# Optimization experiments

Hardware: AMD Instinct MI355X
Metric: run time of the kernel (lower is better)

Reference implementation:

```python
import jax, jax.numpy as jnp
import numpy as np
from jax import lax

K = 3          # kernel (patch size)
D = 64         # MPO bond dimension
F = K * K      # feature dim per patch (k^2 * C, C=1)
S = F          # output-index spacing inside each SMPO
OUT = 10       # final output dimension
B = 128        # batch size
H = 81         # image height = width
SIGMA = 1e-3   # 'random_eye' noise scale


def patch_embed(x, k=K):
    """squeeze_image + trigonometric embedding.
    x: (B, h, w) -> unit vectors (B, N, 2) with N=(h/k)*(w/k).
    Each k*k patch row is embedded as the L2-normalized mean of
    [cos(pi/2 x), sin(pi/2 x)] over its k^2 features."""
    b, h, w = x.shape
    p = x.reshape(b, h // k, k, w // k, k).transpose(0, 1, 3, 2, 4)
    p = p.reshape(b, (h // k) * (w // k), k * k)
    ang = 0.5 * jnp.pi * p
    v = jnp.stack([jnp.cos(ang).mean(-1), jnp.sin(ang).mean(-1)], axis=-1)
    return v / jnp.linalg.norm(v, axis=-1, keepdims=True)


def smpo_layer(v, W_out, W_mid):
    """Spaced MPO applied to a product-state MPS, read out per output site.
    v:      (B, n, 2)  input site vectors (n = J*S sites, output at every S-th)
    W_out:  (J, D, D, 2, F)  output-site tensors (identity baseline baked in)
    W_mid:  (J, S-1, D, D, 2) non-output site tensors; effective matrix is
            M = I + einsum('bp,dep->bde', v, W) ('random_eye' init).
    Output row j = L_j . A_j(v) . R_j where L/R are left/right chain
    environments with the other output indices closed with ones.
    Returns (B, J, F)."""
    b, n, _ = v.shape
    J = W_out.shape[0]
    s = n // J
    eye = jnp.eye(D, dtype=v.dtype)
    vg = v.reshape(b, J, s, 2)
    v_out = vg[:, :, 0, :].transpose(1, 0, 2)        # (J, B, 2)
    v_mid = vg[:, :, 1:, :].transpose(1, 2, 0, 3)    # (J, S-1, B, 2)

    def left_step(l, xs):
        A, vo, Wm, vm = xs
        Lj = l                                       # env left of output site j
        l = jnp.einsum('bd,bp,depf->be', l, vo, A)   # Abar (f summed = ones closure)
        for t in range(s - 1):
            M = eye + jnp.einsum('bp,dep->bde', vm[t], Wm[t])
            l = jnp.einsum('bd,bde->be', l, M)
        return l, Lj

    def right_step(r, xs):
        A, vo, Wm, vm = xs
        for t in reversed(range(s - 1)):
            M = eye + jnp.einsum('bp,dep->bde', vm[t], Wm[t])
            r = jnp.einsum('bde,be->bd', M, r)
        Rj = r                                       # env right of output site j
        r = jnp.einsum('bp,depf,be->bd', vo, A, r)
        return r, Rj

    bnd = jnp.zeros((b, D), v.dtype).at[:, 0].set(1.0)  # bond-1 boundary
    xs = (W_out, v_out, W_mid, v_mid)
    _, L = lax.scan(jax.checkpoint(left_step), bnd, xs)
    _, R = lax.scan(jax.checkpoint(right_step), bnd, xs, reverse=True)
    return jnp.einsum('jbd,jdepf,jbp,jbe->bjf', L, W_out, v_out, R)


def final_layer(x, A0, W_mid):
    """Final SMPO (spacing = n, single output index at site 0), fully
    contracted left-to-right. x: (B, n) -> (B, OUT)."""
    ang = 0.5 * jnp.pi * x
    v = jnp.stack([jnp.cos(ang), jnp.sin(ang)], axis=-1)   # (B, n, 2)
    eye = jnp.eye(D, dtype=x.dtype)
    u = jnp.einsum('bp,epo->beo', v[:, 0], A0[0])          # left boundary e0

    def step(u, xs):
        Wm, vm = xs
        M = eye + jnp.einsum('bp,dep->bde', vm, Wm)
        return jnp.einsum('bdo,bde->beo', u, M), None

    u, _ = lax.scan(jax.checkpoint(step), u, (W_mid, v[:, 1:].transpose(1, 0, 2)))
    return u[:, 0, :]                                      # right boundary e0


def setup_inputs() -> dict:
    key = jax.random.key(0)
    ks = jax.random.split(key, 7)
    eyeD = np.eye(D, dtype=np.float32)

    def wout(k, J):  # identity baseline + noise ('random_eye')
        base = jnp.asarray((0.8 / F) * eyeD[:, :, None, None])
        return base + SIGMA * jax.random.normal(k, (J, D, D, 2, F), jnp.float32)

    def wmid(k, J):
        return SIGMA * jax.random.normal(k, (J, S - 1, D, D, 2), jnp.float32)

    x = jax.random.uniform(ks[0], (B, H, H, 1), jnp.float32)
    Wout0 = wout(ks[1], 81)
    Wmid0 = wmid(ks[2], 81)
    Wout1 = wout(ks[3], 9)
    Wmid1 = wmid(ks[4], 9)
    A0f = jnp.asarray(0.1 * eyeD[:, :, None, None]) + SIGMA * jax.random.normal(
        ks[5], (D, D, 2, OUT), jnp.float32)
    WmidF = SIGMA * jax.random.normal(ks[6], (80, D, D, 2), jnp.float32)
    return {"x": x, "Wout0": Wout0, "Wmid0": Wmid0, "Wout1": Wout1,
            "Wmid1": Wmid1, "A0f": A0f, "WmidF": WmidF}


def reference(x, Wout0, Wmid0, Wout1, Wmid1, A0f, WmidF):
    v0 = patch_embed(x[..., 0])                    # (B, 729, 2)
    h1 = smpo_layer(v0, Wout0, Wmid0)              # (B, 81, 9)
    v1 = patch_embed(h1.reshape(-1, 27, 27))       # (B, 81, 2)
    h2 = smpo_layer(v1, Wout1, Wmid1)              # (B, 9, 9)
    return final_layer(h2.reshape(-1, 81), A0f, WmidF)  # (B, 10)
```

## Files before the change

### kernel.cpp

```cpp
#include <hip/hip_runtime.h>
#include <cstdint>
#include <cstddef>


typedef float    f32x16 __attribute__((ext_vector_type(16)));
typedef _Float16 f16x8  __attribute__((ext_vector_type(8)));
typedef __fp16   fp16x2 __attribute__((ext_vector_type(2)));
typedef _Float16 h2_t   __attribute__((ext_vector_type(2)));
typedef unsigned int uint32x2_t __attribute__((ext_vector_type(2)));
typedef const void __attribute__((address_space(1))) gas_t;
typedef void       __attribute__((address_space(3))) las_t;

union U16  { uint4 u; f16x8 h; };
union B16u { uint32_t u[4]; f16x8 h; };
union H2U  { fp16x2 h; uint32_t u; };

__device__ __forceinline__ uint32_t pkf16(float a, float b){
  H2U z; z.h = __builtin_amdgcn_cvt_pkrtz(a, b); return z.u;
}
__device__ __forceinline__ uint32_t pkmul(uint32_t a, uint32_t b){
  H2U x, y, r; x.u = a; y.u = b;
  r.h = x.h * y.h; return r.u;
}
__device__ __forceinline__ uint32_t packh2(float a, float b){
  union { _Float16 h[2]; uint32_t u; } z;
  z.h[0] = (_Float16)a; z.h[1] = (_Float16)b; return z.u;
}
__device__ __forceinline__ float fdot2f(uint32_t wa, uint32_t wb, float acc){
  union U { uint32_t u; h2_t h; };
  U a, b; a.u = wa; b.u = wb;
  return __builtin_amdgcn_fdot2(a.h, b.h, acc, false);
}

#define REC 17408

__global__ void k_build(const float* __restrict__ Wmid, const float* __restrict__ Wout,
                        char* __restrict__ S, int J, int n, int dirR){
  int tid = blockIdx.x*256 + threadIdx.x;
  if (tid >= n*4096) return;
  int gt = tid >> 12, r = tid & 4095;
  int f = r >> 8, ln = (r >> 2) & 63, dw = r & 3;
  int s = f >> 1, m = f & 1;
  int row = m*32 + (ln & 31);
  int kb = s*16 + (ln >> 5)*8 + dw*2;
  int p = kb >> 6, q = kb & 63;
  int jj = gt/9, pos = gt - jj*9;
  int j = dirR ? (J-1-jj) : jj;
  int outs = dirR ? 8 : 0;
  float w[2];
  #pragma unroll
  for (int k2 = 0; k2 < 2; ++k2){
    int qq = q + k2;
    int d = dirR ? row : qq;
    int e = dirR ? qq : row;
    float val;
    if (pos == outs){
      const float* src = Wout + ((((size_t)j*64 + d)*64 + e)*2 + p)*9;
      val = 0.f;
      #pragma unroll
      for (int ff = 0; ff < 9; ++ff) val += src[ff];
      if (d == e) val -= 0.8f;
    } else {
      int mi = dirR ? (7 - pos) : (pos - 1);
      val = Wmid[((((size_t)j*8 + mi)*64 + d)*64 + e)*2 + p];
    }
    w[k2] = val;
  }
  uint32_t* S32 = (uint32_t*)(S + (size_t)gt*REC);
  S32[f*256 + ln*4 + dw] = packh2(w[0]*256.f, w[1]*256.f);
}

__global__ void k_buildF(const float* __restrict__ Wm, char* __restrict__ S){
  int tid = blockIdx.x*256 + threadIdx.x;
  if (tid >= 80*4096) return;
  int gt = tid >> 12, r = tid & 4095;
  int f = r >> 8, ln = (r >> 2) & 63, dw = r & 3;
  int s = f >> 1, m = f & 1;
  int row = m*32 + (ln & 31);
  int kb = s*16 + (ln >> 5)*8 + dw*2;
  int p = kb >> 6, q = kb & 63;
  float w[2];
  #pragma unroll
  for (int k2 = 0; k2 < 2; ++k2){
    int d = q + k2, e = row;
    w[k2] = Wm[(((size_t)gt*64 + d)*64 + e)*2 + p];
  }
  uint32_t* S32 = (uint32_t*)(S + (size_t)gt*REC);
  S32[f*256 + ln*4 + dw] = packh2(w[0]*256.f, w[1]*256.f);
}

__global__ void k_vrec(const float2* __restrict__ v, char* __restrict__ S,
                       int n, int nv, int mode){
  int tid = blockIdx.x*256 + threadIdx.x;
  if (tid >= n*128) return;
  int gt = tid >> 7, b = tid & 127;
  int site = (mode == 0) ? gt : (mode == 1) ? (n-1-gt) : (gt+1);
  *(float2*)(S + (size_t)gt*REC + 16384 + b*8) = v[(size_t)b*nv + site];
}

__global__ void k_embed(const float* __restrict__ img, int Wd, int PG,
                        float2* __restrict__ outv){
  int tid = blockIdx.x*256 + threadIdx.x;
  int NP = PG*PG;
  if (tid >= 128*NP) return;
  int b = tid / NP, s = tid - b*NP;
  int pi = s / PG, pj = s - pi*PG;
  const float* base = img + (size_t)b*Wd*Wd + (size_t)(3*pi)*Wd + 3*pj;
  float cs = 0.f, sn = 0.f;
  #pragma unroll
  for (int r = 0; r < 3; ++r){
    #pragma unroll
    for (int c = 0; c < 3; ++c){
      float x = base[r*Wd + c];
      float s_, c_; sincosf(1.5707963267948966f*x, &s_, &c_);
      cs += c_; sn += s_;
    }
  }
  cs *= (1.f/9.f); sn *= (1.f/9.f);
  float rn = rsqrtf(cs*cs + sn*sn);
  float2 v; v.x = cs*rn; v.y = sn*rn;
  outv[tid] = v;
}

__device__ __forceinline__ void stage17(const char* g, char* l){
  #pragma unroll
  for (int i = 0; i < 17; ++i)
    __builtin_amdgcn_global_load_lds((gas_t*)(const void*)(g + i*1024),
                                     (las_t*)(void*)(l + i*1024), 16, 0, 0);
}

#define MKBASE(acc, bd) do { \
  uint32_t P0 = pkf16(acc[0],acc[1]),  P1 = pkf16(acc[2],acc[3]); \
  uint32_t P2 = pkf16(acc[4],acc[5]),  P3 = pkf16(acc[6],acc[7]); \
  { uint32x2_t r_ = __builtin_amdgcn_permlane32_swap(P0, P2, false, false); \
    bd[0] = r_[0]; bd[2] = r_[1]; } \
  { uint32x2_t r_ = __builtin_amdgcn_permlane32_swap(P1, P3, false, false); \
    bd[1] = r_[0]; bd[3] = r_[1]; } \
  uint32_t R0 = pkf16(acc[8],acc[9]),   R1 = pkf16(acc[10],acc[11]); \
  uint32_t R2 = pkf16(acc[12],acc[13]), R3 = pkf16(acc[14],acc[15]); \
  { uint32x2_t r_ = __builtin_amdgcn_permlane32_swap(R0, R2, false, false); \
    bd[4] = r_[0]; bd[6] = r_[1]; } \
  { uint32x2_t r_ = __builtin_amdgcn_permlane32_swap(R1, R3, false, false); \
    bd[5] = r_[0]; bd[7] = r_[1]; } \
} while(0)

#define MFMA8(slotp) do { \
  const uint4* fr_ = (const uint4*)(slotp); \
  _Pragma("unroll") \
  for (int s_ = 0; s_ < 8; ++s_){ \
    const int sl_ = s_ & 3; \
    const uint32_t* bb_ = (sl_ < 2) ? bd0 : bd1; \
    const int off_ = (sl_ & 1)*4; \
    const uint32_t scl_ = (s_ < 4) ? px : py; \
    B16u bs_; \
    _Pragma("unroll") \
    for (int dw_ = 0; dw_ < 4; ++dw_) bs_.u[dw_] = pkmul(bb_[off_+dw_], scl_); \
    U16 fa0_, fa1_; \
    fa0_.u = fr_[(2*s_)*64 + ln]; \
    fa1_.u = fr_[(2*s_+1)*64 + ln]; \
    acc0 = __builtin_amdgcn_mfma_f32_32x32x16_f16(fa0_.h, bs_.h, acc0, 0, 0, 0); \
    acc1 = __builtin_amdgcn_mfma_f32_32x32x16_f16(fa1_.h, bs_.h, acc1, 0, 0, 0); \
  } \
} while(0)

#define PROD_SLOOP(buf) do { \
  const uint4* fr = (const uint4*)(buf); \
  _Pragma("unroll") \
  for (int s = 0; s < 8; ++s){ \
    const int sl = s & 3; \
    const uint32_t scl = (s < 4) ? px : py; \
    const int off = (sl & 1)*4; \
    U16 f0, f1; \
    f0.u = fr[(2*s)*64 + ln]; \
    f1.u = fr[(2*s+1)*64 + ln]; \
    { \
      const uint32_t* bb = (sl < 2) ? bl0 : bh0; \
      B16u bs; \
      _Pragma("unroll") \
      for (int dw = 0; dw < 4; ++dw) bs.u[dw] = pkmul(bb[off+dw], scl); \
      a00 = __builtin_amdgcn_mfma_f32_32x32x16_f16(f0.h, bs.h, a00, 0, 0, 0); \
      a10 = __builtin_amdgcn_mfma_f32_32x32x16_f16(f1.h, bs.h, a10, 0, 0, 0); \
    } \
    { \
      const uint32_t* bb = (sl < 2) ? bl1 : bh1; \
      B16u bs; \
      _Pragma("unroll") \
      for (int dw = 0; dw < 4; ++dw) bs.u[dw] = pkmul(bb[off+dw], scl); \
      a01 = __builtin_amdgcn_mfma_f32_32x32x16_f16(f0.h, bs.h, a01, 0, 0, 0); \
      a11 = __builtin_amdgcn_mfma_f32_32x32x16_f16(f1.h, bs.h, a11, 0, 0, 0); \
    } \
  } \
} while(0)

#define PROD_INIT_I() do { \
  _Pragma("unroll") \
  for (int i = 0; i < 16; ++i){ a00[i]=0.f; a01[i]=0.f; a10[i]=0.f; a11[i]=0.f; } \
  if (((i32 >> 2) & 1) == h){ \
    int rr0 = (i32 & 3) | ((i32 >> 3) << 2); \
    _Pragma("unroll") \
    for (int rr = 0; rr < 16; ++rr) \
      if (rr == rr0){ a00[rr] = 1.f; a11[rr] = 1.f; } \
  } \
} while(0)

#define PROD_WRITEOUT(ob, diagc) do { \
  _Pragma("unroll") \
  for (int x = 0; x < 2; ++x){ \
    _Pragma("unroll") \
    for (int y = 0; y < 2; ++y){ \
      const f32x16& A = (x==0) ? (y==0 ? a00 : a01) : (y==0 ? a10 : a11); \
      int C = y*32 + i32; \
      _Pragma("unroll") \
      for (int r = 0; r < 16; ++r){ \
        int R = x*32 + (r & 3) + 8*(r >> 2) + 4*h; \
        float val = (A[r] - ((R == C) ? (diagc) : 0.f))*256.f; \
        float oth = __shfl_xor(val, 1); \
        if (!(ln & 1)){ \
          uint32_t dwv = packh2(val, oth); \
          *(uint32_t*)((ob) + R*128 + ((C*2) ^ ((R & 7) << 4))) = dwv; \
        } \
      } \
    } \
  } \
} while(0)

#define PROD_STEP(t, doalpha) do { \
  uint32_t px = pkf16(vv[t].x*INV, vv[t].x*INV); \
  uint32_t py = pkf16(vv[t].y*INV, vv[t].y*INV); \
  uint32_t bl0[8], bh0[8], bl1[8], bh1[8]; \
  MKBASE(a00, bl0); MKBASE(a10, bh0); \
  MKBASE(a01, bl1); MKBASE(a11, bh1); \
  if (doalpha){ \
    _Pragma("unroll") \
    for (int i = 0; i < 16; ++i){ \
      a00[i] *= alphaC; a01[i] *= alphaC; a10[i] *= alphaC; a11[i] *= alphaC; \
    } \
  } \
  PROD_SLOOP(lds + (size_t)(t)*16384); \
} while(0)

__global__ __launch_bounds__(512, 1) void k_prod(
    const char* __restrict__ sL, const char* __restrict__ sR,
    const float2* __restrict__ v, char* __restrict__ Tn, char* __restrict__ Wn,
    int J){
  __shared__ __align__(16) char lds[9*16384];
  const int ln = threadIdx.x & 63, w = threadIdx.x >> 6;
  const int wid = (blockIdx.x & 7)*(J*4) + (blockIdx.x >> 3);
  const int bg = wid & 15;
  const int pair = wid >> 4;
  const int dir = pair & 1, j = pair >> 1;
  const int b = bg*8 + w;
  const int h = ln >> 5, i32 = ln & 31;
  const float INV = 1.f/256.f;
  const char* stream = dir ? sR : sL;
  const int n = J*9;

  float2 vv[9];
  {
    const float2* vbase = v + (size_t)b*n + j*9;
    #pragma unroll
    for (int t = 0; t < 9; ++t) vv[t] = vbase[dir ? (9 - t) : t];
  }
  const float alphaC = (dir && j == J-1) ? 1.0f : 0.8f*(vv[0].x + vv[0].y);
  if (dir && j == J-1){ vv[0].x = 0.f; vv[0].y = 0.f; }

  auto gtf = [&](int t) -> int {
    int g = dir ? ((J-2-j)*9 + 8 + t) : (j*9 + t);
    return g < 0 ? 0 : g;
  };
  auto stage = [&](int t){
    const char* g0 = stream + (size_t)gtf(t)*REC + (size_t)(2*w)*1024 + (size_t)ln*16;
    char* l0 = lds + (size_t)t*16384;
    __builtin_amdgcn_global_load_lds((gas_t*)(const void*)g0,
                                     (las_t*)(void*)(l0 + 2*w*1024), 16, 0, 0);
    __builtin_amdgcn_global_load_lds((gas_t*)(const void*)(g0 + 1024),
                                     (las_t*)(void*)(l0 + (2*w+1)*1024), 16, 0, 0);
  };

  f32x16 a00, a01, a10, a11;
  PROD_INIT_I();

  stage(0); stage(1); stage(2);
  asm volatile("s_waitcnt vmcnt(0)" ::: "memory");
  __builtin_amdgcn_s_barrier();
  #pragma unroll
  for (int t = 3; t < 9; ++t) stage(t);

  PROD_STEP(0, true);
  PROD_STEP(1, false);
  PROD_STEP(2, false);
  asm volatile("s_waitcnt vmcnt(0)" ::: "memory");
  __builtin_amdgcn_s_barrier();
  #pragma unroll
  for (int t = 3; t < 9; ++t) PROD_STEP(t, false);

  char* ob = (dir ? Wn : Tn) + ((size_t)b*J + j)*8192;
  PROD_WRITEOUT(ob, alphaC);
}

__global__ __launch_bounds__(512, 1) void k_prodF(
    const char* __restrict__ sF, const float2* __restrict__ vF,
    char* __restrict__ GF){
  __shared__ __align__(16) char lds[8*16384];
  const int ln = threadIdx.x & 63, w = threadIdx.x >> 6;
  const int wid = (blockIdx.x & 7)*20 + (blockIdx.x >> 3);
  const int bg = wid & 15, g = wid >> 4;
  const int b = bg*8 + w;
  const int h = ln >> 5, i32 = ln & 31;
  const float INV = 1.f/256.f;
  const float alphaC = 1.0f;

  float2 vv[8];
  {
    const float2* vbase = vF + (size_t)b*81 + g*8 + 1;
    #pragma unroll
    for (int t = 0; t < 8; ++t) vv[t] = vbase[t];
  }
  auto stage = [&](int t){
    const char* g0 = sF + (size_t)(g*8 + t)*REC + (size_t)(2*w)*1024 + (size_t)ln*16;
    char* l0 = lds + (size_t)t*16384;
    __builtin_amdgcn_global_load_lds((gas_t*)(const void*)g0,
                                     (las_t*)(void*)(l0 + 2*w*1024), 16, 0, 0);
    __builtin_amdgcn_global_load_lds((gas_t*)(const void*)(g0 + 1024),
                                     (las_t*)(void*)(l0 + (2*w+1)*1024), 16, 0, 0);
  };

  f32x16 a00, a01, a10, a11;
  PROD_INIT_I();

  stage(0); stage(1); stage(2);
  asm volatile("s_waitcnt vmcnt(0)" ::: "memory");
  __builtin_amdgcn_s_barrier();
  #pragma unroll
  for (int t = 3; t < 8; ++t) stage(t);

  PROD_STEP(0, false);
  PROD_STEP(1, false);
  PROD_STEP(2, false);
  asm volatile("s_waitcnt vmcnt(0)" ::: "memory");
  __builtin_amdgcn_s_barrier();
  #pragma unroll
  for (int t = 3; t < 8; ++t) PROD_STEP(t, false);

  char* ob = GF + ((size_t)b*10 + g)*8192;
  PROD_WRITEOUT(ob, 1.0f);
}

__global__ __launch_bounds__(64, 1) void k_gscan(
    const char* __restrict__ Tn, const char* __restrict__ Wn,
    const float2* __restrict__ v,
    float* __restrict__ Lout, float* __restrict__ Rout, int J){
  __shared__ __align__(16) char slot[4][8192];
  __shared__ __align__(16) float2 vvs[81];
  __shared__ __align__(16) uint32_t pk32[32];
  const int ln = threadIdx.x;
  const int dir = blockIdx.x >> 7;
  const int b = blockIdx.x & 127;
  const float INV = 1.f/256.f;
  const char* P = (dir ? Wn : Tn) + (size_t)b*J*8192;

  for (int g = ln; g < J; g += 64) vvs[g] = v[(size_t)b*(J*9) + (size_t)g*9];

  auto JD = [&](int g){ return dir ? (J-1-g) : g; };
  auto stage8 = [&](int jx, int sl){
    const char* g0 = P + (size_t)jx*8192 + (size_t)ln*16;
    #pragma unroll
    for (int i = 0; i < 8; ++i)
      __builtin_amdgcn_global_load_lds((gas_t*)(const void*)(g0 + i*1024),
                                       (las_t*)(void*)(slot[sl] + i*1024), 16, 0, 0);
  };

  stage8(JD(0), 0);
  stage8(JD(1 < J-1 ? 1 : J-1), 1);
  stage8(JD(2 < J-1 ? 2 : J-1), 2);

  float st = (ln == 0) ? 1.f : 0.f;
  const uint32_t swz = (uint32_t)(ln & 7) << 4;

  #pragma unroll 1
  for (int g = 0; g < J; ++g){
    const int j = JD(g);
    asm volatile("s_waitcnt vmcnt(16)" ::: "memory");
    if (!dir) Lout[((size_t)j*128 + b)*64 + ln] = st;
    {
      int gn = (g+3 > J-1) ? (J-1) : (g+3);
      stage8(JD(gn), (g+3) & 3);
    }

    float c;
    if (dir) c = (j < J-1) ? 0.8f*(vvs[j+1].x + vvs[j+1].y) : 1.0f;
    else     c = 0.8f*(vvs[j].x + vvs[j].y);

    {
      float o = __shfl_xor(st, 1);
      pk32[ln>>1] = (ln & 1) ? packh2(o, st) : packh2(st, o);
    }
    const char* sp = slot[g & 3] + (size_t)ln*128;
    const uint4* lp = (const uint4*)pk32;
    float acc = 0.f;
    #pragma unroll
    for (int m = 0; m < 8; ++m){
      uint4 q = lp[m];
      uint4 ww = *(const uint4*)(sp + ((m*16) ^ swz));
      acc = fdot2f(ww.x, q.x, acc); acc = fdot2f(ww.y, q.y, acc);
      acc = fdot2f(ww.z, q.z, acc); acc = fdot2f(ww.w, q.w, acc);
    }
    st = c*st + acc*INV;
    if (dir) Rout[((size_t)j*128 + b)*64 + ln] = st;
  }
}

__global__ __launch_bounds__(64, 1) void k_fscan(
    const char* __restrict__ GF, const float* __restrict__ A0f,
    const float2* __restrict__ vF, float* __restrict__ outp){
  __shared__ __align__(16) char slot[4][8192];
  __shared__ __align__(16) uint32_t pk[10][32];
  const int ln = threadIdx.x;
  const int b = blockIdx.x;
  const float INV = 1.f/256.f;
  const char* P = GF + (size_t)b*10*8192;

  float2 v0 = vF[(size_t)b*81];
  float u[10];
  #pragma unroll
  for (int o = 0; o < 10; ++o)
    u[o] = v0.x*A0f[(ln*2+0)*10 + o] + v0.y*A0f[(ln*2+1)*10 + o];

  auto stage8 = [&](int g, int sl){
    const char* g0 = P + (size_t)g*8192 + (size_t)ln*16;
    #pragma unroll
    for (int i = 0; i < 8; ++i)
      __builtin_amdgcn_global_load_lds((gas_t*)(const void*)(g0 + i*1024),
                                       (las_t*)(void*)(slot[sl] + i*1024), 16, 0, 0);
  };

  stage8(0, 0);
  stage8(1, 1);
  stage8(2, 2);
  const uint32_t swz = (uint32_t)(ln & 7) << 4;

  #pragma unroll 1
  for (int g = 0; g < 10; ++g){
    asm volatile("s_waitcnt vmcnt(16)" ::: "memory");
    {
      int gn = (g+3 > 9) ? 9 : (g+3);
      stage8(gn, (g+3) & 3);
    }
    #pragma unroll
    for (int o = 0; o < 10; ++o){
      float ot = __shfl_xor(u[o], 1);
      pk[o][ln>>1] = (ln & 1) ? packh2(ot, u[o]) : packh2(u[o], ot);
    }
    const char* sp = slot[g & 3] + (size_t)ln*128;
    uint4 wr[8];
    #pragma unroll
    for (int m = 0; m < 8; ++m) wr[m] = *(const uint4*)(sp + ((m*16) ^ swz));
    #pragma unroll
    for (int o = 0; o < 10; ++o){
      const uint4* lp = (const uint4*)pk[o];
      float acc = 0.f;
      #pragma unroll
      for (int m = 0; m < 8; ++m){
        uint4 q = lp[m];
        acc = fdot2f(wr[m].x, q.x, acc); acc = fdot2f(wr[m].y, q.y, acc);
        acc = fdot2f(wr[m].z, q.z, acc); acc = fdot2f(wr[m].w, q.w, acc);
      }
      u[o] += acc*INV;
    }
  }
  if (ln == 0){
    #pragma unroll
    for (int o = 0; o < 10; ++o) outp[(size_t)b*10 + o] = u[o];
  }
}

__global__ __launch_bounds__(64, 1) void k_scan_m(
    const char* __restrict__ sL, const char* __restrict__ sR,
    float* __restrict__ Lout, float* __restrict__ Rout, int J, int n){
  __shared__ __align__(16) char lds[4*REC];
  const int ln = threadIdx.x;
  const int wg = blockIdx.x;
  const int dir = wg >> 2;
  const int colbase = (wg & 3)*32;
  const char* stream = dir ? sR : sL;
  float* Sout = dir ? Rout : Lout;
  const int outs = dir ? 8 : 0;
  const int b = colbase + (ln & 31);
  const int h4 = (ln >> 5)*4;
  const float INV = 1.f/256.f;

  f32x16 acc0, acc1;
  #pragma unroll
  for (int i = 0; i < 16; ++i){ acc0[i] = 0.f; acc1[i] = 0.f; }
  if (ln < 32) acc0[0] = 1.f;

  const char* gsrc = stream + (size_t)ln*16;
  stage17(gsrc,           lds);
  stage17(gsrc + REC,     lds + REC);
  stage17(gsrc + 2*REC,   lds + 2*REC);

  int pos = 0, jj = 0;
  for (int t = 0; t < n; ++t){
    asm volatile("s_waitcnt vmcnt(34)" ::: "memory");
    const char* slot = lds + (size_t)(t & 3)*REC;
    float2 vv = *(const float2*)(slot + 16384 + b*8);
    int tn = t + 3; if (tn > n-1) tn = n-1;
    stage17(gsrc + (size_t)tn*REC, lds + (size_t)(tn & 3)*REC);

    uint32_t px = pkf16(vv.x*INV, vv.x*INV);
    uint32_t py = pkf16(vv.y*INV, vv.y*INV);
    uint32_t bd0[8], bd1[8];
    MKBASE(acc0, bd0);
    MKBASE(acc1, bd1);

    if (pos == outs){
      int jdx = dir ? (J-1-jj) : jj;
      float* dst = Sout + ((size_t)jdx*128 + b)*64;
      #pragma unroll
      for (int q = 0; q < 4; ++q){
        float4 f0; f0.x = acc0[4*q]; f0.y = acc0[4*q+1]; f0.z = acc0[4*q+2]; f0.w = acc0[4*q+3];
        *(float4*)(dst + 8*q + h4) = f0;
        float4 f1; f1.x = acc1[4*q]; f1.y = acc1[4*q+1]; f1.z = acc1[4*q+2]; f1.w = acc1[4*q+3];
        *(float4*)(dst + 32 + 8*q + h4) = f1;
      }
      float alpha = 0.8f*(vv.x + vv.y);
      #pragma unroll
      for (int i = 0; i < 16; ++i){ acc0[i] *= alpha; acc1[i] *= alpha; }
    }

    MFMA8(slot);

    ++pos; if (pos == 9){ pos = 0; ++jj; }
  }
}

__global__ __launch_bounds__(64, 1) void k_final_m(
    const char* __restrict__ sF, const float* __restrict__ A0f,
    const float2* __restrict__ vF, float* __restrict__ outp){
  __shared__ __align__(16) char lds[4*REC];
  const int ln = threadIdx.x;
  const int wg = blockIdx.x;
  const int o = wg >> 2;
  const int b = (wg & 3)*32 + (ln & 31);
  const int h4 = (ln >> 5)*4;
  const float INV = 1.f/256.f;

  float2 v0 = vF[(size_t)b*81];
  f32x16 acc0, acc1;
  #pragma unroll
  for (int rg = 0; rg < 16; ++rg){
    int row0 = (rg & 3) + 8*(rg >> 2) + h4;
    acc0[rg] = v0.x*A0f[(row0*2+0)*10 + o] + v0.y*A0f[(row0*2+1)*10 + o];
    int row1 = row0 + 32;
    acc1[rg] = v0.x*A0f[(row1*2+0)*10 + o] + v0.y*A0f[(row1*2+1)*10 + o];
  }
  asm volatile("s_waitcnt vmcnt(0)" ::: "memory");

  const char* gsrc = sF + (size_t)ln*16;
  stage17(gsrc,         lds);
  stage17(gsrc + REC,   lds + REC);
  stage17(gsrc + 2*REC, lds + 2*REC);

  const int n = 80;
  for (int t = 0; t < n; ++t){
    asm volatile("s_waitcnt vmcnt(34)" ::: "memory");
    const char* slot = lds + (size_t)(t & 3)*REC;
    float2 vv = *(const float2*)(slot + 16384 + b*8);
    int tn = t + 3; if (tn > n-1) tn = n-1;
    stage17(gsrc + (size_t)tn*REC, lds + (size_t)(tn & 3)*REC);

    uint32_t px = pkf16(vv.x*INV, vv.x*INV);
    uint32_t py = pkf16(vv.y*INV, vv.y*INV);
    uint32_t bd0[8], bd1[8];
    MKBASE(acc0, bd0);
    MKBASE(acc1, bd1);
    MFMA8(slot);
  }
  if (ln < 32) outp[(size_t)b*10 + o] = acc0[0];
}

template<bool EMB>
__global__ __launch_bounds__(256) void k_out(
    const float* __restrict__ Wout, const float* __restrict__ Lbuf,
    const float* __restrict__ Rbuf, const float2* __restrict__ v, int n,
    float* __restrict__ hout, float2* __restrict__ vF){
  __shared__ float tile[8][64][20];
  __shared__ float Lsh[32][65];
  const int j = blockIdx.x, bh = blockIdx.y;
  const int q = threadIdx.x >> 5, bl = threadIdx.x & 31;
  const int b = bh*32 + bl;
  for (int idx = threadIdx.x; idx < 32*64; idx += 256){
    int r = idx >> 6, d = idx & 63;
    Lsh[r][d] = Lbuf[((size_t)j*128 + bh*32 + r)*64 + d];
  }
  float Rr[8];
  {
    const float4* Rp = (const float4*)(Rbuf + ((size_t)j*128 + b)*64 + q*8);
    ((float4*)Rr)[0] = Rp[0];
    ((float4*)Rr)[1] = Rp[1];
  }
  float acc[18];
  #pragma unroll
  for (int k = 0; k < 18; ++k) acc[k] = 0.f;
  __syncthreads();
  for (int c = 0; c < 8; ++c){
    #pragma unroll
    for (int k = 0; k < 2; ++k){
      int pi = threadIdx.x*2 + k;
      int d8 = pi >> 6, e = pi & 63;
      const float* src = Wout + ((size_t)(j*64 + c*8 + d8)*64 + e)*18;
      float* dst = &tile[d8][e][0];
      #pragma unroll
      for (int mm = 0; mm < 18; ++mm) dst[mm] = src[mm];
    }
    __syncthreads();
    #pragma unroll 1
    for (int d8 = 0; d8 < 8; ++d8){
      float lw = Lsh[bl][c*8 + d8];
      #pragma unroll
      for (int i = 0; i < 8; ++i){
        int e = q*8 + i;
        float wbe = lw * Rr[i];
        const float* tp = &tile[d8][e][0];
        float4 t0 = *(const float4*)(tp);
        float4 t1 = *(const float4*)(tp+4);
        float4 t2 = *(const float4*)(tp+8);
        float4 t3 = *(const float4*)(tp+12);
        float2 t4 = *(const float2*)(tp+16);
        acc[0]  += wbe*t0.x; acc[1]  += wbe*t0.y; acc[2]  += wbe*t0.z; acc[3]  += wbe*t0.w;
        acc[4]  += wbe*t1.x; acc[5]  += wbe*t1.y; acc[6]  += wbe*t1.z; acc[7]  += wbe*t1.w;
        acc[8]  += wbe*t2.x; acc[9]  += wbe*t2.y; acc[10] += wbe*t2.z; acc[11] += wbe*t2.w;
        acc[12] += wbe*t3.x; acc[13] += wbe*t3.y; acc[14] += wbe*t3.z; acc[15] += wbe*t3.w;
        acc[16] += wbe*t4.x; acc[17] += wbe*t4.y;
      }
    }
    __syncthreads();
  }
  float* red = &tile[0][0][0];
  #pragma unroll
  for (int k = 0; k < 18; ++k) red[((size_t)q*32 + bl)*20 + k] = acc[k];
  __syncthreads();
  if (q == 0){
    float s[18];
    #pragma unroll
    for (int k = 0; k < 18; ++k){
      float t = 0.f;
      #pragma unroll
      for (int g = 0; g < 8; ++g) t += red[((size_t)g*32 + bl)*20 + k];
      s[k] = t;
    }
    float2 vo = v[(size_t)b*n + j*9];
    #pragma unroll
    for (int f = 0; f < 9; ++f){
      float val = vo.x*s[f] + vo.y*s[9+f];
      if (EMB){
        float s_, c_; sincosf(1.5707963267948966f*val, &s_, &c_);
        float2 e2; e2.x = c_; e2.y = s_;
        vF[(size_t)b*81 + j*9 + f] = e2;
      } else {
        hout[(size_t)b*729 + j*9 + f] = val;
      }
    }
  }
}

extern "C" void kernel_launch(void* const* d_in, const int* in_sizes, int n_in,
                              void* d_out, int out_size, void* d_ws, size_t ws_size,
                              hipStream_t stream){
  const float* x     = (const float*)d_in[0];
  const float* Wout0 = (const float*)d_in[1];
  const float* Wmid0 = (const float*)d_in[2];
  const float* Wout1 = (const float*)d_in[3];
  const float* Wmid1 = (const float*)d_in[4];
  const float* A0f   = (const float*)d_in[5];
  const float* WmidF = (const float*)d_in[6];
  float* outp = (float*)d_out;

  char* ws = (char*)d_ws;
  size_t off = 0;
  auto alloc = [&](size_t bytes) -> char* {
    char* p = ws + off;
    off = (off + bytes + 255) & ~(size_t)255;
    return p;
  };
  char* S0L = alloc((size_t)729*REC);
  char* S0R = alloc((size_t)729*REC);
  char* S1L = alloc((size_t)81*REC);
  char* S1R = alloc((size_t)81*REC);
  char* SF  = alloc((size_t)80*REC);
  float2* v0 = (float2*)alloc((size_t)128*729*8);
  float2* v1 = (float2*)alloc((size_t)128*81*8);
  float2* vF = (float2*)alloc((size_t)128*81*8);
  float* L0 = (float*)alloc((size_t)81*128*64*4);
  float* R0 = (float*)alloc((size_t)81*128*64*4);
  float* L1 = (float*)alloc((size_t)9*128*64*4);
  float* R1 = (float*)alloc((size_t)9*128*64*4);
  float* h1 = (float*)alloc((size_t)128*729*4);
  char* Tn1 = alloc((size_t)128*81*8192);
  char* Wn1 = alloc((size_t)128*81*8192);
  size_t need_r7 = off;
  char* Tn2 = alloc((size_t)128*9*8192);
  char* Wn2 = alloc((size_t)128*9*8192);
  char* GF  = alloc((size_t)128*10*8192);
  size_t need_full = off;
  bool full = (ws_size >= need_full);
  bool grp1 = (ws_size >= need_r7);
  (void)in_sizes; (void)n_in; (void)out_size;

  k_build <<<1296,  256, 0, stream>>>(Wmid1, Wout1, S1L, 9, 81, 0);
  k_build <<<1296,  256, 0, stream>>>(Wmid1, Wout1, S1R, 9, 81, 1);
  k_buildF<<<1280,  256, 0, stream>>>(WmidF, SF);
  k_build<<<11664, 256, 0, stream>>>(Wmid0, Wout0, S0L, 81, 729, 0);
  k_build<<<11664, 256, 0, stream>>>(Wmid0, Wout0, S0R, 81, 729, 1);

  k_embed<<<365, 256, 0, stream>>>(x, 81, 27, v0);
  if (grp1){
    k_prod <<<2592, 512, 0, stream>>>(S0L, S0R, v0, Tn1, Wn1, 81);
    k_gscan<<<256, 64, 0, stream>>>(Tn1, Wn1, v0, L0, R0, 81);
  } else {
    k_vrec <<<365, 256, 0, stream>>>(v0, S0L, 729, 729, 0);
    k_vrec <<<365, 256, 0, stream>>>(v0, S0R, 729, 729, 1);
    k_scan_m<<<8, 64, 0, stream>>>(S0L, S0R, L0, R0, 81, 729);
  }
  k_out<false><<<dim3(81,4), 256, 0, stream>>>(Wout0, L0, R0, v0, 729, h1, (float2*)nullptr);

  k_embed<<<41, 256, 0, stream>>>(h1, 27, 9, v1);
  if (full){
    k_prod <<<288, 512, 0, stream>>>(S1L, S1R, v1, Tn2, Wn2, 9);
    k_gscan<<<256, 64, 0, stream>>>(Tn2, Wn2, v1, L1, R1, 9);
  } else {
    k_vrec <<<41, 256, 0, stream>>>(v1, S1L, 81, 81, 0);
    k_vrec <<<41, 256, 0, stream>>>(v1, S1R, 81, 81, 1);
    k_scan_m<<<8, 64, 0, stream>>>(S1L, S1R, L1, R1, 9, 81);
  }
  k_out<true><<<dim3(9,4), 256, 0, stream>>>(Wout1, L1, R1, v1, 81, (float*)nullptr, vF);

  if (full){
    k_prodF<<<160, 512, 0, stream>>>(SF, vF, GF);
    k_fscan<<<128, 64, 0, stream>>>(GF, A0f, vF, outp);
  } else {
    k_vrec <<<40, 256, 0, stream>>>(vF, SF, 80, 81, 2);
    k_final_m<<<40, 64, 0, stream>>>(SF, A0f, vF, outp);
  }
}
```

Measured before the change: 502.6 us.

## Replace full-LDS staging with a 3-slot ring buffer in product kernels

The product kernels now stage weight tiles through a 3-slot LDS ring with prefetch distance 2 and a per-step waitcnt and barrier. Before, they staged all 8 or 9 tiles into LDS in two bulk phases. This cuts LDS use per block from 144KB to 48KB and overlaps each load with compute more evenly. In exchange it adds a barrier every step and issues redundant loads of the last tile at the tail. Launch bounds still force one block per SM, so the lower LDS use does not raise occupancy.

```diff
diff --git a/kernel.cpp b/kernel.cpp
--- a/kernel.cpp
+++ b/kernel.cpp
@@ -224,7 +224,7 @@
   } \
 } while(0)
 
-#define PROD_STEP(t, doalpha) do { \
+#define PROD_STEP(t, doalpha, bufp) do { \
   uint32_t px = pkf16(vv[t].x*INV, vv[t].x*INV); \
   uint32_t py = pkf16(vv[t].y*INV, vv[t].y*INV); \
   uint32_t bl0[8], bh0[8], bl1[8], bh1[8]; \
@@ -236,14 +236,14 @@
       a00[i] *= alphaC; a01[i] *= alphaC; a10[i] *= alphaC; a11[i] *= alphaC; \
     } \
   } \
-  PROD_SLOOP(lds + (size_t)(t)*16384); \
+  PROD_SLOOP(bufp); \
 } while(0)
 
 __global__ __launch_bounds__(512, 1) void k_prod(
     const char* __restrict__ sL, const char* __restrict__ sR,
     const float2* __restrict__ v, char* __restrict__ Tn, char* __restrict__ Wn,
     int J){
-  __shared__ __align__(16) char lds[9*16384];
+  __shared__ __align__(16) char lds[3][16384];
   const int ln = threadIdx.x & 63, w = threadIdx.x >> 6;
   const int wid = (blockIdx.x & 7)*(J*4) + (blockIdx.x >> 3);
   const int bg = wid & 15;
@@ -268,31 +268,30 @@
     int g = dir ? ((J-2-j)*9 + 8 + t) : (j*9 + t);
     return g < 0 ? 0 : g;
   };
-  auto stage = [&](int t){
+  auto stage = [&](int t, int sl){
     const char* g0 = stream + (size_t)gtf(t)*REC + (size_t)(2*w)*1024 + (size_t)ln*16;
-    char* l0 = lds + (size_t)t*16384;
     __builtin_amdgcn_global_load_lds((gas_t*)(const void*)g0,
-                                     (las_t*)(void*)(l0 + 2*w*1024), 16, 0, 0);
+                                     (las_t*)(void*)(lds[sl] + 2*w*1024), 16, 0, 0);
     __builtin_amdgcn_global_load_lds((gas_t*)(const void*)(g0 + 1024),
-                                     (las_t*)(void*)(l0 + (2*w+1)*1024), 16, 0, 0);
+                                     (las_t*)(void*)(lds[sl] + (2*w+1)*1024), 16, 0, 0);
   };
 
   f32x16 a00, a01, a10, a11;
   PROD_INIT_I();
 
-  stage(0); stage(1); stage(2);
-  asm volatile("s_waitcnt vmcnt(0)" ::: "memory");
-  __builtin_amdgcn_s_barrier();
-  #pragma unroll
-  for (int t = 3; t < 9; ++t) stage(t);
-
-  PROD_STEP(0, true);
-  PROD_STEP(1, false);
-  PROD_STEP(2, false);
-  asm volatile("s_waitcnt vmcnt(0)" ::: "memory");
-  __builtin_amdgcn_s_barrier();
-  #pragma unroll
-  for (int t = 3; t < 9; ++t) PROD_STEP(t, false);
+  stage(0, 0);
+  stage(1, 1);
+  #pragma unroll
+  for (int t = 0; t < 9; ++t){
+    asm volatile("s_waitcnt vmcnt(2)" ::: "memory");
+    __builtin_amdgcn_s_barrier();
+    {
+      int tn = (t+2 > 8) ? 8 : (t+2);
+      stage(tn, (t+2) % 3);
+    }
+    if (t == 0){ PROD_STEP(0, true, lds[0]); }
+    else       { PROD_STEP(t, false, lds[t % 3]); }
+  }
 
   char* ob = (dir ? Wn : Tn) + ((size_t)b*J + j)*8192;
   PROD_WRITEOUT(ob, alphaC);
@@ -301,7 +300,7 @@
 __global__ __launch_bounds__(512, 1) void k_prodF(
     const char* __restrict__ sF, const float2* __restrict__ vF,
     char* __restrict__ GF){
-  __shared__ __align__(16) char lds[8*16384];
+  __shared__ __align__(16) char lds[3][16384];
   const int ln = threadIdx.x & 63, w = threadIdx.x >> 6;
   const int wid = (blockIdx.x & 7)*20 + (blockIdx.x >> 3);
   const int bg = wid & 15, g = wid >> 4;
@@ -316,31 +315,29 @@
     #pragma unroll
     for (int t = 0; t < 8; ++t) vv[t] = vbase[t];
   }
-  auto stage = [&](int t){
+  auto stage = [&](int t, int sl){
     const char* g0 = sF + (size_t)(g*8 + t)*REC + (size_t)(2*w)*1024 + (size_t)ln*16;
-    char* l0 = lds + (size_t)t*16384;
     __builtin_amdgcn_global_load_lds((gas_t*)(const void*)g0,
-                                     (las_t*)(void*)(l0 + 2*w*1024), 16, 0, 0);
+                                     (las_t*)(void*)(lds[sl] + 2*w*1024), 16, 0, 0);
     __builtin_amdgcn_global_load_lds((gas_t*)(const void*)(g0 + 1024),
-                                     (las_t*)(void*)(l0 + (2*w+1)*1024), 16, 0, 0);
+                                     (las_t*)(void*)(lds[sl] + (2*w+1)*1024), 16, 0, 0);
   };
 
   f32x16 a00, a01, a10, a11;
   PROD_INIT_I();
 
-  stage(0); stage(1); stage(2);
-  asm volatile("s_waitcnt vmcnt(0)" ::: "memory");
-  __builtin_amdgcn_s_barrier();
-  #pragma unroll
-  for (int t = 3; t < 8; ++t) stage(t);
-
-  PROD_STEP(0, false);
-  PROD_STEP(1, false);
-  PROD_STEP(2, false);
-  asm volatile("s_waitcnt vmcnt(0)" ::: "memory");
-  __builtin_amdgcn_s_barrier();
-  #pragma unroll
-  for (int t = 3; t < 8; ++t) PROD_STEP(t, false);
+  stage(0, 0);
+  stage(1, 1);
+  #pragma unroll
+  for (int t = 0; t < 8; ++t){
+    asm volatile("s_waitcnt vmcnt(2)" ::: "memory");
+    __builtin_amdgcn_s_barrier();
+    {
+      int tn = (t+2 > 7) ? 7 : (t+2);
+      stage(tn, (t+2) % 3);
+    }
+    PROD_STEP(t, false, lds[t % 3]);
+  }
 
   char* ob = GF + ((size_t)b*10 + g)*8192;
   PROD_WRITEOUT(ob, 1.0f);
```

Measured after the change: 470.9 us. -6.3%, faster.
